# Optimization experiments

Hardware: AMD Instinct MI355X
Metric: run time of the kernel (lower is better)

## Reference

```python
import jax, jax.numpy as jnp
import numpy as np

B, N, T, D, E, M = 8, 512, 64, 128, 32, 3


def _norm(v):
    return v / jnp.clip(jnp.linalg.norm(v, axis=-1, keepdims=True), 1e-12)


def setup_inputs() -> dict:
    key = jax.random.key(0)
    ks = jax.random.split(key, 14)
    s = 0.05
    x = jax.random.normal(ks[0], (B, N, T, 1), jnp.float32)
    # set_prior: binarized adjacency + self loops, row-normalized
    a = (jax.random.uniform(ks[1], (N, N)) > 0.95).astype(jnp.float32) + jnp.eye(N, dtype=jnp.float32)
    prior = a / jnp.clip(a.sum(1, keepdims=True), 1e-8)
    # orthogonal queries, as in torch __init__ (QR of zero-padded randn)
    rng = np.random.default_rng(0)
    qs = []
    for _ in range(M):
        pad = np.zeros((D, D), np.float32)
        pad[:E] = rng.standard_normal((E, D)).astype(np.float32) * 0.1
        q, _ = np.linalg.qr(pad)
        qs.append(q[:E])
    return {
        "x": x,
        "prior": prior,
        "proj_W": jax.random.normal(ks[2], (D, 1), jnp.float32) * s,
        "proj_b": jnp.zeros((D,), jnp.float32),
        "W_ih": jax.random.normal(ks[3], (3 * D, D), jnp.float32) * s,
        "W_hh": jax.random.normal(ks[4], (3 * D, D), jnp.float32) * s,
        "b_ih": jnp.zeros((3 * D,), jnp.float32),
        "b_hh": jnp.zeros((3 * D,), jnp.float32),
        "space_W": jax.random.normal(ks[5], (M, D, D), jnp.float32) * s,
        "space_b": jnp.zeros((M, D), jnp.float32),
        "router_W": jax.random.normal(ks[6], (M, 2 * D), jnp.float32) * s,
        "router_b": jnp.zeros((M,), jnp.float32),
        "out_W": jax.random.normal(ks[7], (1, D), jnp.float32) * s,
        "out_b": jnp.zeros((1,), jnp.float32),
        "prior_logit": jnp.array(1.0, jnp.float32),
        "queries": jnp.asarray(np.stack(qs)),  # [M, E, D]
    }


def reference(x, prior, proj_W, proj_b, W_ih, W_hh, b_ih, b_hh,
              space_W, space_b, router_W, router_b, out_W, out_b,
              prior_logit, queries):
    b, n, t, _ = x.shape
    d = proj_b.shape[0]
    m, e, _ = queries.shape
    # proj(x.permute(0,2,1,3)).reshape(B*N, T, D)  (faithful reshape of [B,T,N,D])
    hp = jnp.transpose(x, (0, 2, 1, 3)) @ proj_W.T + proj_b  # [B,T,N,D]
    seq = hp.reshape(b * n, t, d)
    xs = jnp.swapaxes(seq, 0, 1)  # [T, BN, D]

    def gru_step(h, xt):
        gi = xt @ W_ih.T + b_ih
        gh = h @ W_hh.T + b_hh
        ir, iz, i_n = jnp.split(gi, 3, axis=-1)
        hr, hz, h_n = jnp.split(gh, 3, axis=-1)
        r = jax.nn.sigmoid(ir + hr)
        z = jax.nn.sigmoid(iz + hz)
        ng = jnp.tanh(i_n + r * h_n)
        return (1.0 - z) * ng + z * h, None

    h, _ = jax.lax.scan(gru_step, jnp.zeros((b * n, d), x.dtype), xs)
    h = h.reshape(b, n, d)

    stats = jnp.concatenate([h.mean(1), jnp.std(h, axis=1, ddof=1)], axis=-1)  # torch std is unbiased
    probs = jax.nn.softmax(stats @ router_W.T + router_b, axis=-1)  # [B,M]

    z_prior = jnp.einsum('ij,bjd->bid', prior, h)

    hs = _norm(jnp.einsum('bnd,mkd->bmnk', h, space_W) + space_b[None, :, None, :])  # [B,M,N,D]
    q = _norm(queries)  # [M,E,D]
    scores = jnp.einsum('bmnd,med->bmen', hs, q)  # [B,M,E,N] (topk over N axis)
    k = min(n, max(4, int(n * 0.05)))
    vals, idx = jax.lax.top_k(scores, k)  # [B,M,E,k]
    w = jax.nn.softmax(vals / 0.7, axis=-1)
    H = jnp.zeros((b, m, e, n), h.dtype).at[
        jnp.arange(b)[:, None, None, None],
        jnp.arange(m)[None, :, None, None],
        jnp.arange(e)[None, None, :, None],
        idx,
    ].set(w)  # [B,M,E,N], transposed layout of torch's [B,N,E]

    Hmix = jnp.einsum('bmen,bm->ben', H, probs)  # [B,E,N] == torch Hmix^T
    edge = jnp.einsum('ben,bnd->bed', Hmix, h)   # Hmix^T @ h
    z_learn = jnp.einsum('ben,bed->bnd', Hmix, edge)  # Hmix @ edge

    alpha = jax.nn.sigmoid(prior_logit)
    out = (alpha * z_prior + (1.0 - alpha) * z_learn) @ out_W.T + out_b  # [B,N,1]
    return out.squeeze(-1), probs
```

## Files before the change

### kernel.cpp

```cpp
#include <hip/hip_runtime.h>
#include <math.h>

#define OFF_U      0
#define OFF_C      384
#define OFF_QWHI   768
#define OFF_QWLO   6912
#define OFF_H      13056
#define OFF_PROBS  537344
#define OFF_HV     537376
#define OFF_SCORES 541472
#define OFF_HMIX   934688
#define OFF_WHI    1066016
#define OFF_SHI    1115168
#define OFF_SLO    1139744
#define OFF_STATS  1164320
#define OFF_EV     1229856
#define OFF_QB     1230112

typedef short bf16x8 __attribute__((ext_vector_type(8)));
typedef float f32x4 __attribute__((ext_vector_type(4)));

union U8 { unsigned short s[8]; bf16x8 v; uint4 u4; };

__device__ __forceinline__ unsigned short bf16_rtn(float f) {
  unsigned int u = __float_as_uint(f);
  return (unsigned short)((u + 0x7FFFu + ((u >> 16) & 1u)) >> 16);
}
__device__ __forceinline__ float bf16_f(unsigned short h) {
  return __uint_as_float(((unsigned int)h) << 16);
}

__global__ __launch_bounds__(256) void prep_kernel(const float* __restrict__ Wih,
                                                   const float* __restrict__ projW,
                                                   const float* __restrict__ projb,
                                                   const float* __restrict__ bih,
                                                   const float* __restrict__ queries,
                                                   const float* __restrict__ Whh,
                                                   const float* __restrict__ spaceW,
                                                   const float* __restrict__ spaceb,
                                                   float* __restrict__ ws) {
  const int bid = blockIdx.x, tid = threadIdx.x;
  const int wave = tid >> 6, lane = tid & 63;
  if (bid < 96) {
    int r = bid * 4 + wave;
    float w0 = Wih[r * 128 + lane], w1 = Wih[r * 128 + 64 + lane];
    float u = w0 * projW[lane] + w1 * projW[64 + lane];
    float c = w0 * projb[lane] + w1 * projb[64 + lane];
    for (int off = 32; off; off >>= 1) {
      u += __shfl_xor(u, off);
      c += __shfl_xor(c, off);
    }
    if (lane == 0) {
      ws[OFF_U + r] = u;
      ws[OFF_C + r] = c + bih[r];
    }
  } else if (bid < 112) {
    unsigned short* WHI = (unsigned short*)(ws + OFF_WHI);
    int base = (bid - 96) * 3072;
    for (int i = tid; i < 3072; i += 256)
      WHI[base + i] = bf16_rtn(Whh[base + i]);
  } else if (bid < 128) {
    unsigned short* SHI = (unsigned short*)(ws + OFF_SHI);
    unsigned short* SLO = (unsigned short*)(ws + OFF_SLO);
    int base = (bid - 112) * 3072;
    for (int i = tid; i < 3072; i += 256) {
      float w = spaceW[base + i];
      unsigned short hi = bf16_rtn(w);
      SHI[base + i] = hi;
      SLO[base + i] = bf16_rtn(w - bf16_f(hi));
    }
  } else if (bid < 224) {
    int qi = bid - 128;
    int m = qi >> 5, e = qi & 31;
    __shared__ float invS, qdS;
    const float* qrow = queries + (m * 32 + e) * 128;
    if (wave == 0) {
      float v0 = qrow[lane], v1 = qrow[64 + lane];
      float ss = v0 * v0 + v1 * v1;
      for (int off = 32; off; off >>= 1) ss += __shfl_xor(ss, off);
      if (lane == 0) invS = 1.f / fmaxf(sqrtf(ss), 1e-12f);
    } else if (wave == 1) {
      float v = qrow[lane] * spaceb[m * 128 + lane] +
                qrow[64 + lane] * spaceb[m * 128 + 64 + lane];
      for (int off = 32; off; off >>= 1) v += __shfl_xor(v, off);
      if (lane == 0) qdS = v;
    }
    __syncthreads();
    if (tid < 128) {
      int din = tid;
      float acc = 0.f;
      for (int dout = 0; dout < 128; ++dout)
        acc += qrow[dout] * spaceW[m * 16384 + dout * 128 + din];
      acc *= invS;
      unsigned short hi = bf16_rtn(acc);
      ((unsigned short*)(ws + OFF_QWHI))[(m * 32 + e) * 128 + din] = hi;
      ((unsigned short*)(ws + OFF_QWLO))[(m * 32 + e) * 128 + din] =
          bf16_rtn(acc - bf16_f(hi));
    }
    if (tid == 255) ws[OFF_QB + m * 32 + e] = qdS * invS;
  } else {
    ws[OFF_EV + tid] = 0.f;
  }
}

__global__ __launch_bounds__(512, 2) void gru_kernel(const float* __restrict__ x,
                                                     const float* __restrict__ bhh,
                                                     const float* __restrict__ outW,
                                                     float* __restrict__ ws) {
  __shared__ __align__(16) unsigned short hB[2][16 * 17 * 8];
  __shared__ float xsAll[16 * 65];
  __shared__ float hFin[16 * 132];

  const int tid = threadIdx.x, wave = tid >> 6, lane = tid & 63;
  const int q = lane >> 4, s15 = lane & 15;
  const int d = wave * 16 + s15;
  const unsigned short* WHI = (const unsigned short*)(ws + OFF_WHI);

  {
    float4 z4 = make_float4(0.f, 0.f, 0.f, 0.f);
    float4* hm4 = (float4*)(ws + OFF_HMIX);
    if (tid < 128) hm4[blockIdx.x * 128 + tid] = z4;
  }

  bf16x8 Bh[3][4];
#pragma unroll
  for (int t = 0; t < 3; ++t) {
    int row = (wave + 8 * t) * 16 + s15;
#pragma unroll
    for (int c = 0; c < 4; ++c)
      Bh[t][c] = *(const bf16x8*)&WHI[row * 128 + c * 32 + q * 8];
  }
  const float ur = ws[OFF_U + d],       uz = ws[OFF_U + 128 + d], un = ws[OFF_U + 256 + d];
  const float cr = ws[OFF_C + d] + bhh[d];
  const float cz = ws[OFF_C + 128 + d] + bhh[128 + d];
  const float cn = ws[OFF_C + 256 + d];
  const float bj2 = bhh[256 + d];

  const int seq0 = blockIdx.x * 16;
  for (int i = tid; i < 1024; i += 512) {
    int s = i >> 6, tt = i & 63;
    int r = (seq0 + s) * 64 + tt;
    xsAll[s * 65 + tt] = x[((r >> 15) * 512 + (r & 511)) * 64 + ((r >> 9) & 63)];
  }
  for (int i = tid; i < 2176; i += 512) hB[0][i] = 0;
  __syncthreads();

  float hreg[4] = {0.f, 0.f, 0.f, 0.f};
  const int g = d >> 3, e = d & 7;

  for (int t = 0; t < 64; ++t) {
    const int rb = t & 1, wb = rb ^ 1;
    f32x4 acc0 = {0.f, 0.f, 0.f, 0.f};
    f32x4 acc1 = {0.f, 0.f, 0.f, 0.f};
    f32x4 acc2 = {0.f, 0.f, 0.f, 0.f};
#pragma unroll
    for (int c = 0; c < 4; ++c) {
      bf16x8 A = *(const bf16x8*)&hB[rb][((c * 4 + q) * 17 + s15) * 8];
      acc0 = __builtin_amdgcn_mfma_f32_16x16x32_bf16(A, Bh[0][c], acc0, 0, 0, 0);
      acc1 = __builtin_amdgcn_mfma_f32_16x16x32_bf16(A, Bh[1][c], acc1, 0, 0, 0);
      acc2 = __builtin_amdgcn_mfma_f32_16x16x32_bf16(A, Bh[2][c], acc2, 0, 0, 0);
    }
    float xsv[4];
#pragma unroll
    for (int r = 0; r < 4; ++r) xsv[r] = xsAll[(q * 4 + r) * 65 + t];
#pragma unroll
    for (int r = 0; r < 4; ++r) {
      int s = q * 4 + r;
      float gr = fmaf(xsv[r], ur, cr + acc0[r]);
      float gz = fmaf(xsv[r], uz, cz + acc1[r]);
      float gn = fmaf(xsv[r], un, cn);
      float hn = acc2[r] + bj2;
      float rr = __builtin_amdgcn_rcpf(1.f + __expf(-gr));
      float zm = __builtin_amdgcn_rcpf(1.f + __expf(gz));
      float a = fmaf(rr, hn, gn);
      float ng = 1.f - 2.f * __builtin_amdgcn_rcpf(__expf(2.f * a) + 1.f);
      float hv = fmaf(zm, ng - hreg[r], hreg[r]);
      hreg[r] = hv;
      hB[wb][(g * 17 + s) * 8 + e] = bf16_rtn(hv);
    }
    __syncthreads();
  }

#pragma unroll
  for (int r = 0; r < 4; ++r) hFin[(q * 4 + r) * 132 + d] = hreg[r];
  __syncthreads();
  float* h_out = ws + OFF_H;
#pragma unroll
  for (int p = 0; p < 4; ++p) {
    int item = tid + p * 512;
    int s = item >> 7, dd = item & 127;
    h_out[(seq0 + s) * 128 + dd] = hFin[s * 132 + dd];
  }
  for (int s = wave * 2; s < wave * 2 + 2; ++s) {
    float a = hFin[s * 132 + lane] * outW[lane] + hFin[s * 132 + 64 + lane] * outW[64 + lane];
    for (int off = 32; off; off >>= 1) a += __shfl_xor(a, off);
    if (lane == 0) ws[OFF_HV + seq0 + s] = a;
  }
  if (tid < 128) {
    float s = 0.f, q2 = 0.f;
#pragma unroll
    for (int sI = 0; sI < 16; ++sI) {
      float v = hFin[sI * 132 + tid];
      s += v; q2 += v * v;
    }
    ws[OFF_STATS + blockIdx.x * 256 + tid] = s;
    ws[OFF_STATS + blockIdx.x * 256 + 128 + tid] = q2;
  }
}

__global__ __launch_bounds__(256) void scores_kernel(const float* __restrict__ spaceb,
                                                     const float* __restrict__ routerW,
                                                     const float* __restrict__ routerb,
                                                     float* __restrict__ ws,
                                                     float* __restrict__ d_out) {
  const int bid = blockIdx.x;
  const int chunk = bid & 15, m = (bid >> 4) % 3, b = bid / 48;
  const int n0 = chunk * 32;
  const int tid = threadIdx.x, wave = tid >> 6, lane = tid & 63;
  const int q = lane >> 4, s15 = lane & 15;

  __shared__ __align__(16) unsigned short sHi[16 * 33 * 8];
  __shared__ __align__(16) unsigned short sLo[16 * 33 * 8];
  __shared__ float hsL[32 * 132];
  __shared__ float biasL[128];
  __shared__ float invnL[32];
  __shared__ float qbL[32];

  const float* hG = ws + OFF_H;
  const unsigned short* SHI = (const unsigned short*)(ws + OFF_SHI);
  const unsigned short* SLO = (const unsigned short*)(ws + OFF_SLO);
  const unsigned short* QWHI = (const unsigned short*)(ws + OFF_QWHI);
  const unsigned short* QWLO = (const unsigned short*)(ws + OFF_QWLO);

  if (tid < 128) biasL[tid] = spaceb[m * 128 + tid];
  else if (tid < 160) qbL[tid - 128] = ws[OFF_QB + m * 32 + (tid - 128)];
  {
    int nn = tid >> 3, kc = tid & 7;
    const float* row = &hG[(b * 512 + n0 + nn) * 128 + kc * 16];
    U8 ph0, pl0, ph1, pl1;
#pragma unroll
    for (int j = 0; j < 8; ++j) {
      float v = row[j];
      unsigned short hi = bf16_rtn(v);
      ph0.s[j] = hi; pl0.s[j] = bf16_rtn(v - bf16_f(hi));
    }
#pragma unroll
    for (int j = 0; j < 8; ++j) {
      float v = row[8 + j];
      unsigned short hi = bf16_rtn(v);
      ph1.s[j] = hi; pl1.s[j] = bf16_rtn(v - bf16_f(hi));
    }
    int g0 = kc * 2;
    *(uint4*)&sHi[(g0 * 33 + nn) * 8] = ph0.u4;
    *(uint4*)&sLo[(g0 * 33 + nn) * 8] = pl0.u4;
    *(uint4*)&sHi[((g0 + 1) * 33 + nn) * 8] = ph1.u4;
    *(uint4*)&sLo[((g0 + 1) * 33 + nn) * 8] = pl1.u4;
  }
  __syncthreads();

  const int nt = wave >> 1;
  const int half = wave & 1;
  const int dt0 = half * 4;
  f32x4 acc[4] = {{0.f,0.f,0.f,0.f},{0.f,0.f,0.f,0.f},{0.f,0.f,0.f,0.f},{0.f,0.f,0.f,0.f}};
  f32x4 accS = {0.f, 0.f, 0.f, 0.f};
#pragma unroll
  for (int c = 0; c < 4; ++c) {
    bf16x8 Ahi = *(const bf16x8*)&sHi[((c * 4 + q) * 33 + nt * 16 + s15) * 8];
    bf16x8 Alo = *(const bf16x8*)&sLo[((c * 4 + q) * 33 + nt * 16 + s15) * 8];
#pragma unroll
    for (int i = 0; i < 4; ++i) {
      int row = m * 16384 + ((dt0 + i) * 16 + s15) * 128 + c * 32 + q * 8;
      bf16x8 Bhi = *(const bf16x8*)&SHI[row];
      bf16x8 Blo = *(const bf16x8*)&SLO[row];
      acc[i] = __builtin_amdgcn_mfma_f32_16x16x32_bf16(Ahi, Bhi, acc[i], 0, 0, 0);
      acc[i] = __builtin_amdgcn_mfma_f32_16x16x32_bf16(Alo, Bhi, acc[i], 0, 0, 0);
      acc[i] = __builtin_amdgcn_mfma_f32_16x16x32_bf16(Ahi, Blo, acc[i], 0, 0, 0);
    }
    {
      int row = (m * 32 + half * 16 + s15) * 128 + c * 32 + q * 8;
      bf16x8 Qhi = *(const bf16x8*)&QWHI[row];
      bf16x8 Qlo = *(const bf16x8*)&QWLO[row];
      accS = __builtin_amdgcn_mfma_f32_16x16x32_bf16(Ahi, Qhi, accS, 0, 0, 0);
      accS = __builtin_amdgcn_mfma_f32_16x16x32_bf16(Alo, Qhi, accS, 0, 0, 0);
      accS = __builtin_amdgcn_mfma_f32_16x16x32_bf16(Ahi, Qlo, accS, 0, 0, 0);
    }
  }
#pragma unroll
  for (int i = 0; i < 4; ++i) {
    int dcol = (dt0 + i) * 16 + s15;
    float bb = biasL[dcol];
#pragma unroll
    for (int r = 0; r < 4; ++r)
      hsL[(nt * 16 + q * 4 + r) * 132 + dcol] = acc[i][r] + bb;
  }
  __syncthreads();

  {
    int n = tid >> 3, kc = tid & 7;
    float ss = 0.f;
#pragma unroll
    for (int d4 = 0; d4 < 4; ++d4) {
      float4 v = *(const float4*)&hsL[n * 132 + kc * 16 + d4 * 4];
      ss += v.x * v.x + v.y * v.y + v.z * v.z + v.w * v.w;
    }
    ss += __shfl_xor(ss, 1); ss += __shfl_xor(ss, 2); ss += __shfl_xor(ss, 4);
    if (kc == 0) invnL[n] = 1.f / fmaxf(sqrtf(ss), 1e-12f);
  }
  __syncthreads();

  {
    int e = half * 16 + s15;
    float qb = qbL[e];
    int nb = nt * 16 + q * 4;
    float4 o;
    o.x = (accS[0] + qb) * invnL[nb + 0];
    o.y = (accS[1] + qb) * invnL[nb + 1];
    o.z = (accS[2] + qb) * invnL[nb + 2];
    o.w = (accS[3] + qb) * invnL[nb + 3];
    *(float4*)&ws[OFF_SCORES + ((b * 3 + m) * 32 + e) * 512 + n0 + nb] = o;
  }

  if ((bid % 48) == 0) {
    __syncthreads();
    float* st = hsL;
    float* lgS = hsL + 256;
    if (tid < 128) {
      float s = 0.f, q2 = 0.f;
      const float* base = ws + OFF_STATS + b * 32 * 256;
      for (int j = 0; j < 32; ++j) {
        s += base[j * 256 + tid];
        q2 += base[j * 256 + 128 + tid];
      }
      float mean = s * (1.f / 512.f);
      float var = (q2 - 512.f * mean * mean) * (1.f / 511.f);
      st[tid] = mean;
      st[128 + tid] = sqrtf(fmaxf(var, 0.f));
    }
    __syncthreads();
    if (tid < 3) {
      float acc2 = routerb[tid];
      for (int k = 0; k < 256; ++k) acc2 += st[k] * routerW[tid * 256 + k];
      lgS[tid] = acc2;
    }
    __syncthreads();
    if (tid == 0) {
      float mx = fmaxf(lgS[0], fmaxf(lgS[1], lgS[2]));
      float e0 = expf(lgS[0] - mx), e1 = expf(lgS[1] - mx), e2 = expf(lgS[2] - mx);
      float inv = 1.f / (e0 + e1 + e2);
      ws[OFF_PROBS + b * 3 + 0] = e0 * inv;
      ws[OFF_PROBS + b * 3 + 1] = e1 * inv;
      ws[OFF_PROBS + b * 3 + 2] = e2 * inv;
      d_out[4096 + b * 3 + 0] = e0 * inv;
      d_out[4096 + b * 3 + 1] = e1 * inv;
      d_out[4096 + b * 3 + 2] = e2 * inv;
    }
  }
}

__global__ __launch_bounds__(256) void topk_kernel(float* __restrict__ ws) {
  const int row0 = blockIdx.x * 4;
  const int b = row0 / 96;
  const int tid = threadIdx.x, wave = tid >> 6, lane = tid & 63;
  __shared__ float hvL[512];
  hvL[tid] = ws[OFF_HV + b * 512 + tid];
  hvL[256 + tid] = ws[OFF_HV + b * 512 + 256 + tid];
  __syncthreads();

  int row = row0 + wave;
  int m = (row / 32) % 3, e = row & 31;
  const float* sc = ws + OFF_SCORES + row * 512;
  float prob = ws[OFF_PROBS + b * 3 + m];

  float v[8];
#pragma unroll
  for (int j = 0; j < 8; ++j) v[j] = sc[j * 64 + lane];

  float selv = 0.f; int seli = 0; float maxv = 0.f;
  for (int it = 0; it < 25; ++it) {
    float bv = v[0]; int bj = 0;
#pragma unroll
    for (int j = 1; j < 8; ++j)
      if (v[j] > bv) { bv = v[j]; bj = j; }
    int bidx = bj * 64 + lane;
    for (int off = 32; off; off >>= 1) {
      float ov = __shfl_xor(bv, off);
      int oi = __shfl_xor(bidx, off);
      if (ov > bv || (ov == bv && oi < bidx)) { bv = ov; bidx = oi; }
    }
    if (lane == (bidx & 63)) v[bidx >> 6] = -INFINITY;
    if (it == 0) maxv = bv;
    if (lane == it) { selv = bv; seli = bidx; }
  }
  float ex = (lane < 25) ? __expf((selv - maxv) * (1.f / 0.7f)) : 0.f;
  float den = ex;
  for (int off = 32; off; off >>= 1) den += __shfl_xor(den, off);
  float w = prob * ex / den;
  if (lane < 25)
    atomicAdd(&ws[OFF_HMIX + (b * 32 + e) * 512 + seli], w);
  float evc = (lane < 25) ? w * hvL[seli] : 0.f;
  for (int off = 32; off; off >>= 1) evc += __shfl_xor(evc, off);
  if (lane == 0) atomicAdd(&ws[OFF_EV + b * 32 + e], evc);
}

__global__ __launch_bounds__(512) void final_kernel(const float* __restrict__ prior,
                                                    const float* __restrict__ outb,
                                                    const float* __restrict__ plog,
                                                    float* __restrict__ ws,
                                                    float* __restrict__ d_out) {
  const int bid = blockIdx.x;
  const int b = bid >> 4, ch = bid & 15;
  const int tid = threadIdx.x, wave = tid >> 6, lane = tid & 63;
  __shared__ float hvL[512], evL[32];
  hvL[tid] = ws[OFF_HV + b * 512 + tid];
  if (tid < 32) evL[tid] = ws[OFF_EV + b * 32 + tid];
  __syncthreads();
  float alpha = 1.f / (1.f + expf(-plog[0]));
  float ob = outb[0];
#pragma unroll
  for (int i = 0; i < 4; ++i) {
    int n = ch * 32 + wave * 4 + i;
    const float* pr = prior + n * 512;
    float s1 = 0.f;
#pragma unroll
    for (int j = 0; j < 8; ++j) s1 += pr[j * 64 + lane] * hvL[j * 64 + lane];
    float s2 = 0.f;
    if (lane < 32) s2 = ws[OFF_HMIX + (b * 32 + lane) * 512 + n] * evL[lane];
    float a = alpha * s1 + (1.f - alpha) * s2;
    for (int off = 32; off; off >>= 1) a += __shfl_xor(a, off);
    if (lane == 0) d_out[b * 512 + n] = a + ob;
  }
}

extern "C" void kernel_launch(void* const* d_in, const int* in_sizes, int n_in,
                              void* d_out, int out_size, void* d_ws, size_t ws_size,
                              hipStream_t stream) {
  const float* x       = (const float*)d_in[0];
  const float* prior   = (const float*)d_in[1];
  const float* projW   = (const float*)d_in[2];
  const float* projb   = (const float*)d_in[3];
  const float* Wih     = (const float*)d_in[4];
  const float* Whh     = (const float*)d_in[5];
  const float* bih     = (const float*)d_in[6];
  const float* bhh     = (const float*)d_in[7];
  const float* spaceW  = (const float*)d_in[8];
  const float* spaceb  = (const float*)d_in[9];
  const float* routerW = (const float*)d_in[10];
  const float* routerb = (const float*)d_in[11];
  const float* outW    = (const float*)d_in[12];
  const float* outb    = (const float*)d_in[13];
  const float* plog    = (const float*)d_in[14];
  const float* queries = (const float*)d_in[15];
  float* ws  = (float*)d_ws;
  float* out = (float*)d_out;

  prep_kernel<<<225, 256, 0, stream>>>(Wih, projW, projb, bih, queries, Whh,
                                       spaceW, spaceb, ws);
  gru_kernel<<<256, 512, 0, stream>>>(x, bhh, outW, ws);
  scores_kernel<<<384, 256, 0, stream>>>(spaceb, routerW, routerb, ws, out);
  topk_kernel<<<192, 256, 0, stream>>>(ws);
  final_kernel<<<128, 512, 0, stream>>>(prior, outb, plog, ws, out);
}
```

Before: 174.9 us.

## Fuse scores, topk and final into one kernel with grid-wide spin barriers

Merges the scores, top-k and final kernels into a single persistent 384-block kernel that separates the phases with atomic-counter spin barriers instead of kernel launches. The spaceW splitting, query-weight precompute and EV/sync-counter zeroing move out of the prep kernel into extra blocks appended to the GRU launch, so prep shrinks to the GRU-weight work. The aim is to cut launch gaps and inter-kernel drain time. The spin barriers assume all 384 blocks are co-resident, which risks deadlock if they are not, and they add atomic polling cost.

```diff
diff --git a/kernel.cpp b/kernel.cpp
--- a/kernel.cpp
+++ b/kernel.cpp
@@ -7,6 +7,7 @@
 #define OFF_QWLO   6912
 #define OFF_H      13056
 #define OFF_PROBS  537344
+#define OFF_SYNC   537368
 #define OFF_HV     537376
 #define OFF_SCORES 541472
 #define OFF_HMIX   934688
@@ -30,14 +31,23 @@
   return __uint_as_float(((unsigned int)h) << 16);
 }
 
+__device__ __forceinline__ void spin_sync(unsigned* ctr, unsigned target, int tid) {
+  __threadfence();
+  __syncthreads();
+  if (tid == 0) {
+    __hip_atomic_fetch_add(ctr, 1u, __ATOMIC_ACQ_REL, __HIP_MEMORY_SCOPE_AGENT);
+    while (__hip_atomic_load(ctr, __ATOMIC_ACQUIRE, __HIP_MEMORY_SCOPE_AGENT) < target)
+      __builtin_amdgcn_s_sleep(4);
+  }
+  __syncthreads();
+  __threadfence();
+}
+
 __global__ __launch_bounds__(256) void prep_kernel(const float* __restrict__ Wih,
                                                    const float* __restrict__ projW,
                                                    const float* __restrict__ projb,
                                                    const float* __restrict__ bih,
-                                                   const float* __restrict__ queries,
                                                    const float* __restrict__ Whh,
-                                                   const float* __restrict__ spaceW,
-                                                   const float* __restrict__ spaceb,
                                                    float* __restrict__ ws) {
   const int bid = blockIdx.x, tid = threadIdx.x;
   const int wave = tid >> 6, lane = tid & 63;
@@ -54,64 +64,76 @@
       ws[OFF_U + r] = u;
       ws[OFF_C + r] = c + bih[r];
     }
-  } else if (bid < 112) {
+  } else {
     unsigned short* WHI = (unsigned short*)(ws + OFF_WHI);
     int base = (bid - 96) * 3072;
     for (int i = tid; i < 3072; i += 256)
       WHI[base + i] = bf16_rtn(Whh[base + i]);
-  } else if (bid < 128) {
-    unsigned short* SHI = (unsigned short*)(ws + OFF_SHI);
-    unsigned short* SLO = (unsigned short*)(ws + OFF_SLO);
-    int base = (bid - 112) * 3072;
-    for (int i = tid; i < 3072; i += 256) {
-      float w = spaceW[base + i];
-      unsigned short hi = bf16_rtn(w);
-      SHI[base + i] = hi;
-      SLO[base + i] = bf16_rtn(w - bf16_f(hi));
-    }
-  } else if (bid < 224) {
-    int qi = bid - 128;
-    int m = qi >> 5, e = qi & 31;
-    __shared__ float invS, qdS;
-    const float* qrow = queries + (m * 32 + e) * 128;
-    if (wave == 0) {
-      float v0 = qrow[lane], v1 = qrow[64 + lane];
-      float ss = v0 * v0 + v1 * v1;
-      for (int off = 32; off; off >>= 1) ss += __shfl_xor(ss, off);
-      if (lane == 0) invS = 1.f / fmaxf(sqrtf(ss), 1e-12f);
-    } else if (wave == 1) {
-      float v = qrow[lane] * spaceb[m * 128 + lane] +
-                qrow[64 + lane] * spaceb[m * 128 + 64 + lane];
-      for (int off = 32; off; off >>= 1) v += __shfl_xor(v, off);
-      if (lane == 0) qdS = v;
-    }
-    __syncthreads();
-    if (tid < 128) {
-      int din = tid;
-      float acc = 0.f;
-      for (int dout = 0; dout < 128; ++dout)
-        acc += qrow[dout] * spaceW[m * 16384 + dout * 128 + din];
-      acc *= invS;
-      unsigned short hi = bf16_rtn(acc);
-      ((unsigned short*)(ws + OFF_QWHI))[(m * 32 + e) * 128 + din] = hi;
-      ((unsigned short*)(ws + OFF_QWLO))[(m * 32 + e) * 128 + din] =
-          bf16_rtn(acc - bf16_f(hi));
-    }
-    if (tid == 255) ws[OFF_QB + m * 32 + e] = qdS * invS;
-  } else {
-    ws[OFF_EV + tid] = 0.f;
   }
 }
 
 __global__ __launch_bounds__(512, 2) void gru_kernel(const float* __restrict__ x,
                                                      const float* __restrict__ bhh,
                                                      const float* __restrict__ outW,
+                                                     const float* __restrict__ spaceW,
+                                                     const float* __restrict__ spaceb,
+                                                     const float* __restrict__ queries,
                                                      float* __restrict__ ws) {
   __shared__ __align__(16) unsigned short hB[2][16 * 17 * 8];
   __shared__ float xsAll[16 * 65];
   __shared__ float hFin[16 * 132];
+  __shared__ float invS, qdS;
 
   const int tid = threadIdx.x, wave = tid >> 6, lane = tid & 63;
+
+  if (blockIdx.x >= 256) {
+    const int xb = blockIdx.x - 256;
+    if (xb < 16) {
+      unsigned short* SHI = (unsigned short*)(ws + OFF_SHI);
+      unsigned short* SLO = (unsigned short*)(ws + OFF_SLO);
+      int base = xb * 3072;
+      for (int i = tid; i < 3072; i += 512) {
+        float w = spaceW[base + i];
+        unsigned short hi = bf16_rtn(w);
+        SHI[base + i] = hi;
+        SLO[base + i] = bf16_rtn(w - bf16_f(hi));
+      }
+    } else if (xb < 112) {
+      int qi = xb - 16;
+      int m = qi >> 5, e = qi & 31;
+      const float* qrow = queries + (m * 32 + e) * 128;
+      if (wave == 0) {
+        float v0 = qrow[lane], v1 = qrow[64 + lane];
+        float ss = v0 * v0 + v1 * v1;
+        for (int off = 32; off; off >>= 1) ss += __shfl_xor(ss, off);
+        if (lane == 0) invS = 1.f / fmaxf(sqrtf(ss), 1e-12f);
+      } else if (wave == 1) {
+        float v = qrow[lane] * spaceb[m * 128 + lane] +
+                  qrow[64 + lane] * spaceb[m * 128 + 64 + lane];
+        for (int off = 32; off; off >>= 1) v += __shfl_xor(v, off);
+        if (lane == 0) qdS = v;
+      }
+      __syncthreads();
+      if (tid < 128) {
+        int din = tid;
+        float acc = 0.f;
+        for (int dout = 0; dout < 128; ++dout)
+          acc += qrow[dout] * spaceW[m * 16384 + dout * 128 + din];
+        acc *= invS;
+        unsigned short hi = bf16_rtn(acc);
+        ((unsigned short*)(ws + OFF_QWHI))[(m * 32 + e) * 128 + din] = hi;
+        ((unsigned short*)(ws + OFF_QWLO))[(m * 32 + e) * 128 + din] =
+            bf16_rtn(acc - bf16_f(hi));
+      }
+      if (tid == 0) ws[OFF_QB + m * 32 + e] = qdS * invS;
+    } else {
+      if (tid < 256) ws[OFF_EV + tid] = 0.f;
+      if (tid == 256) ((unsigned*)(ws + OFF_SYNC))[0] = 0u;
+      if (tid == 257) ((unsigned*)(ws + OFF_SYNC))[1] = 0u;
+    }
+    return;
+  }
+
   const int q = lane >> 4, s15 = lane & 15;
   const int d = wave * 16 + s15;
   const unsigned short* WHI = (const unsigned short*)(ws + OFF_WHI);
@@ -208,14 +230,15 @@
   }
 }
 
-__global__ __launch_bounds__(256) void scores_kernel(const float* __restrict__ spaceb,
-                                                     const float* __restrict__ routerW,
-                                                     const float* __restrict__ routerb,
-                                                     float* __restrict__ ws,
-                                                     float* __restrict__ d_out) {
+__global__ __launch_bounds__(256) void megatail_kernel(const float* __restrict__ spaceb,
+                                                       const float* __restrict__ routerW,
+                                                       const float* __restrict__ routerb,
+                                                       const float* __restrict__ prior,
+                                                       const float* __restrict__ outb,
+                                                       const float* __restrict__ plog,
+                                                       float* __restrict__ ws,
+                                                       float* __restrict__ d_out) {
   const int bid = blockIdx.x;
-  const int chunk = bid & 15, m = (bid >> 4) % 3, b = bid / 48;
-  const int n0 = chunk * 32;
   const int tid = threadIdx.x, wave = tid >> 6, lane = tid & 63;
   const int q = lane >> 4, s15 = lane & 15;
 
@@ -226,208 +249,204 @@
   __shared__ float invnL[32];
   __shared__ float qbL[32];
 
-  const float* hG = ws + OFF_H;
-  const unsigned short* SHI = (const unsigned short*)(ws + OFF_SHI);
-  const unsigned short* SLO = (const unsigned short*)(ws + OFF_SLO);
-  const unsigned short* QWHI = (const unsigned short*)(ws + OFF_QWHI);
-  const unsigned short* QWLO = (const unsigned short*)(ws + OFF_QWLO);
-
-  if (tid < 128) biasL[tid] = spaceb[m * 128 + tid];
-  else if (tid < 160) qbL[tid - 128] = ws[OFF_QB + m * 32 + (tid - 128)];
+  unsigned* ctr = (unsigned*)(ws + OFF_SYNC);
+
   {
-    int nn = tid >> 3, kc = tid & 7;
-    const float* row = &hG[(b * 512 + n0 + nn) * 128 + kc * 16];
-    U8 ph0, pl0, ph1, pl1;
-#pragma unroll
-    for (int j = 0; j < 8; ++j) {
-      float v = row[j];
-      unsigned short hi = bf16_rtn(v);
-      ph0.s[j] = hi; pl0.s[j] = bf16_rtn(v - bf16_f(hi));
-    }
-#pragma unroll
-    for (int j = 0; j < 8; ++j) {
-      float v = row[8 + j];
-      unsigned short hi = bf16_rtn(v);
-      ph1.s[j] = hi; pl1.s[j] = bf16_rtn(v - bf16_f(hi));
-    }
-    int g0 = kc * 2;
-    *(uint4*)&sHi[(g0 * 33 + nn) * 8] = ph0.u4;
-    *(uint4*)&sLo[(g0 * 33 + nn) * 8] = pl0.u4;
-    *(uint4*)&sHi[((g0 + 1) * 33 + nn) * 8] = ph1.u4;
-    *(uint4*)&sLo[((g0 + 1) * 33 + nn) * 8] = pl1.u4;
-  }
-  __syncthreads();
-
-  const int nt = wave >> 1;
-  const int half = wave & 1;
-  const int dt0 = half * 4;
-  f32x4 acc[4] = {{0.f,0.f,0.f,0.f},{0.f,0.f,0.f,0.f},{0.f,0.f,0.f,0.f},{0.f,0.f,0.f,0.f}};
-  f32x4 accS = {0.f, 0.f, 0.f, 0.f};
-#pragma unroll
-  for (int c = 0; c < 4; ++c) {
-    bf16x8 Ahi = *(const bf16x8*)&sHi[((c * 4 + q) * 33 + nt * 16 + s15) * 8];
-    bf16x8 Alo = *(const bf16x8*)&sLo[((c * 4 + q) * 33 + nt * 16 + s15) * 8];
+    const int chunk = bid & 15, m = (bid >> 4) % 3, b = bid / 48;
+    const int n0 = chunk * 32;
+    const float* hG = ws + OFF_H;
+    const unsigned short* SHI = (const unsigned short*)(ws + OFF_SHI);
+    const unsigned short* SLO = (const unsigned short*)(ws + OFF_SLO);
+    const unsigned short* QWHI = (const unsigned short*)(ws + OFF_QWHI);
+    const unsigned short* QWLO = (const unsigned short*)(ws + OFF_QWLO);
+
+    if (tid < 128) biasL[tid] = spaceb[m * 128 + tid];
+    else if (tid < 160) qbL[tid - 128] = ws[OFF_QB + m * 32 + (tid - 128)];
+    {
+      int nn = tid >> 3, kc = tid & 7;
+      const float* row = &hG[(b * 512 + n0 + nn) * 128 + kc * 16];
+      U8 ph0, pl0, ph1, pl1;
+#pragma unroll
+      for (int j = 0; j < 8; ++j) {
+        float v = row[j];
+        unsigned short hi = bf16_rtn(v);
+        ph0.s[j] = hi; pl0.s[j] = bf16_rtn(v - bf16_f(hi));
+      }
+#pragma unroll
+      for (int j = 0; j < 8; ++j) {
+        float v = row[8 + j];
+        unsigned short hi = bf16_rtn(v);
+        ph1.s[j] = hi; pl1.s[j] = bf16_rtn(v - bf16_f(hi));
+      }
+      int g0 = kc * 2;
+      *(uint4*)&sHi[(g0 * 33 + nn) * 8] = ph0.u4;
+      *(uint4*)&sLo[(g0 * 33 + nn) * 8] = pl0.u4;
+      *(uint4*)&sHi[((g0 + 1) * 33 + nn) * 8] = ph1.u4;
+      *(uint4*)&sLo[((g0 + 1) * 33 + nn) * 8] = pl1.u4;
+    }
+    __syncthreads();
+
+    const int nt = wave >> 1;
+    const int half = wave & 1;
+    const int dt0 = half * 4;
+    f32x4 acc[4] = {{0.f,0.f,0.f,0.f},{0.f,0.f,0.f,0.f},{0.f,0.f,0.f,0.f},{0.f,0.f,0.f,0.f}};
+    f32x4 accS = {0.f, 0.f, 0.f, 0.f};
+#pragma unroll
+    for (int c = 0; c < 4; ++c) {
+      bf16x8 Ahi = *(const bf16x8*)&sHi[((c * 4 + q) * 33 + nt * 16 + s15) * 8];
+      bf16x8 Alo = *(const bf16x8*)&sLo[((c * 4 + q) * 33 + nt * 16 + s15) * 8];
+#pragma unroll
+      for (int i = 0; i < 4; ++i) {
+        int row = m * 16384 + ((dt0 + i) * 16 + s15) * 128 + c * 32 + q * 8;
+        bf16x8 Bhi = *(const bf16x8*)&SHI[row];
+        bf16x8 Blo = *(const bf16x8*)&SLO[row];
+        acc[i] = __builtin_amdgcn_mfma_f32_16x16x32_bf16(Ahi, Bhi, acc[i], 0, 0, 0);
+        acc[i] = __builtin_amdgcn_mfma_f32_16x16x32_bf16(Alo, Bhi, acc[i], 0, 0, 0);
+        acc[i] = __builtin_amdgcn_mfma_f32_16x16x32_bf16(Ahi, Blo, acc[i], 0, 0, 0);
+      }
+      {
+        int row = (m * 32 + half * 16 + s15) * 128 + c * 32 + q * 8;
+        bf16x8 Qhi = *(const bf16x8*)&QWHI[row];
+        bf16x8 Qlo = *(const bf16x8*)&QWLO[row];
+        accS = __builtin_amdgcn_mfma_f32_16x16x32_bf16(Ahi, Qhi, accS, 0, 0, 0);
+        accS = __builtin_amdgcn_mfma_f32_16x16x32_bf16(Alo, Qhi, accS, 0, 0, 0);
+        accS = __builtin_amdgcn_mfma_f32_16x16x32_bf16(Ahi, Qlo, accS, 0, 0, 0);
+      }
+    }
 #pragma unroll
     for (int i = 0; i < 4; ++i) {
-      int row = m * 16384 + ((dt0 + i) * 16 + s15) * 128 + c * 32 + q * 8;
-      bf16x8 Bhi = *(const bf16x8*)&SHI[row];
-      bf16x8 Blo = *(const bf16x8*)&SLO[row];
-      acc[i] = __builtin_amdgcn_mfma_f32_16x16x32_bf16(Ahi, Bhi, acc[i], 0, 0, 0);
-      acc[i] = __builtin_amdgcn_mfma_f32_16x16x32_bf16(Alo, Bhi, acc[i], 0, 0, 0);
-      acc[i] = __builtin_amdgcn_mfma_f32_16x16x32_bf16(Ahi, Blo, acc[i], 0, 0, 0);
-    }
+      int dcol = (dt0 + i) * 16 + s15;
+      float bb = biasL[dcol];
+#pragma unroll
+      for (int r = 0; r < 4; ++r)
+        hsL[(nt * 16 + q * 4 + r) * 132 + dcol] = acc[i][r] + bb;
+    }
+    __syncthreads();
+
     {
-      int row = (m * 32 + half * 16 + s15) * 128 + c * 32 + q * 8;
-      bf16x8 Qhi = *(const bf16x8*)&QWHI[row];
-      bf16x8 Qlo = *(const bf16x8*)&QWLO[row];
-      accS = __builtin_amdgcn_mfma_f32_16x16x32_bf16(Ahi, Qhi, accS, 0, 0, 0);
-      accS = __builtin_amdgcn_mfma_f32_16x16x32_bf16(Alo, Qhi, accS, 0, 0, 0);
-      accS = __builtin_amdgcn_mfma_f32_16x16x32_bf16(Ahi, Qlo, accS, 0, 0, 0);
-    }
-  }
-#pragma unroll
-  for (int i = 0; i < 4; ++i) {
-    int dcol = (dt0 + i) * 16 + s15;
-    float bb = biasL[dcol];
-#pragma unroll
-    for (int r = 0; r < 4; ++r)
-      hsL[(nt * 16 + q * 4 + r) * 132 + dcol] = acc[i][r] + bb;
-  }
-  __syncthreads();
+      int n = tid >> 3, kc = tid & 7;
+      float ss = 0.f;
+#pragma unroll
+      for (int d4 = 0; d4 < 4; ++d4) {
+        float4 v = *(const float4*)&hsL[n * 132 + kc * 16 + d4 * 4];
+        ss += v.x * v.x + v.y * v.y + v.z * v.z + v.w * v.w;
+      }
+      ss += __shfl_xor(ss, 1); ss += __shfl_xor(ss, 2); ss += __shfl_xor(ss, 4);
+      if (kc == 0) invnL[n] = 1.f / fmaxf(sqrtf(ss), 1e-12f);
+    }
+    __syncthreads();
+
+    {
+      int e = half * 16 + s15;
+      float qb = qbL[e];
+      int nb = nt * 16 + q * 4;
+      float4 o;
+      o.x = (accS[0] + qb) * invnL[nb + 0];
+      o.y = (accS[1] + qb) * invnL[nb + 1];
+      o.z = (accS[2] + qb) * invnL[nb + 2];
+      o.w = (accS[3] + qb) * invnL[nb + 3];
+      *(float4*)&ws[OFF_SCORES + ((b * 3 + m) * 32 + e) * 512 + n0 + nb] = o;
+    }
+
+    if ((bid % 48) == 0) {
+      __syncthreads();
+      float* st = hsL;
+      float* lgS = hsL + 256;
+      if (tid < 128) {
+        float s = 0.f, q2 = 0.f;
+        const float* base = ws + OFF_STATS + b * 32 * 256;
+        for (int j = 0; j < 32; ++j) {
+          s += base[j * 256 + tid];
+          q2 += base[j * 256 + 128 + tid];
+        }
+        float mean = s * (1.f / 512.f);
+        float var = (q2 - 512.f * mean * mean) * (1.f / 511.f);
+        st[tid] = mean;
+        st[128 + tid] = sqrtf(fmaxf(var, 0.f));
+      }
+      __syncthreads();
+      if (tid < 3) {
+        float acc2 = routerb[tid];
+        for (int k = 0; k < 256; ++k) acc2 += st[k] * routerW[tid * 256 + k];
+        lgS[tid] = acc2;
+      }
+      __syncthreads();
+      if (tid == 0) {
+        float mx = fmaxf(lgS[0], fmaxf(lgS[1], lgS[2]));
+        float e0 = expf(lgS[0] - mx), e1 = expf(lgS[1] - mx), e2 = expf(lgS[2] - mx);
+        float inv = 1.f / (e0 + e1 + e2);
+        ws[OFF_PROBS + b * 3 + 0] = e0 * inv;
+        ws[OFF_PROBS + b * 3 + 1] = e1 * inv;
+        ws[OFF_PROBS + b * 3 + 2] = e2 * inv;
+        d_out[4096 + b * 3 + 0] = e0 * inv;
+        d_out[4096 + b * 3 + 1] = e1 * inv;
+        d_out[4096 + b * 3 + 2] = e2 * inv;
+      }
+    }
+  }
+
+  spin_sync(&ctr[0], 384u, tid);
 
   {
-    int n = tid >> 3, kc = tid & 7;
-    float ss = 0.f;
-#pragma unroll
-    for (int d4 = 0; d4 < 4; ++d4) {
-      float4 v = *(const float4*)&hsL[n * 132 + kc * 16 + d4 * 4];
-      ss += v.x * v.x + v.y * v.y + v.z * v.z + v.w * v.w;
-    }
-    ss += __shfl_xor(ss, 1); ss += __shfl_xor(ss, 2); ss += __shfl_xor(ss, 4);
-    if (kc == 0) invnL[n] = 1.f / fmaxf(sqrtf(ss), 1e-12f);
-  }
-  __syncthreads();
+    const int b = bid / 48;
+    for (int i = tid; i < 512; i += 256) hsL[i] = ws[OFF_HV + b * 512 + i];
+    __syncthreads();
+    if (wave < 2) {
+      int row = bid * 2 + wave;
+      int m = (row / 32) % 3, e = row & 31;
+      const float* sc = ws + OFF_SCORES + row * 512;
+      float prob = ws[OFF_PROBS + b * 3 + m];
+      float v[8];
+#pragma unroll
+      for (int j = 0; j < 8; ++j) v[j] = sc[j * 64 + lane];
+      float selv = 0.f; int seli = 0; float maxv = 0.f;
+      for (int it = 0; it < 25; ++it) {
+        float bv = v[0]; int bj = 0;
+#pragma unroll
+        for (int j = 1; j < 8; ++j)
+          if (v[j] > bv) { bv = v[j]; bj = j; }
+        int bidx = bj * 64 + lane;
+        for (int off = 32; off; off >>= 1) {
+          float ov = __shfl_xor(bv, off);
+          int oi = __shfl_xor(bidx, off);
+          if (ov > bv || (ov == bv && oi < bidx)) { bv = ov; bidx = oi; }
+        }
+        if (lane == (bidx & 63)) v[bidx >> 6] = -INFINITY;
+        if (it == 0) maxv = bv;
+        if (lane == it) { selv = bv; seli = bidx; }
+      }
+      float ex = (lane < 25) ? __expf((selv - maxv) * (1.f / 0.7f)) : 0.f;
+      float den = ex;
+      for (int off = 32; off; off >>= 1) den += __shfl_xor(den, off);
+      float w = prob * ex / den;
+      if (lane < 25)
+        atomicAdd(&ws[OFF_HMIX + (b * 32 + e) * 512 + seli], w);
+      float evc = (lane < 25) ? w * hsL[seli] : 0.f;
+      for (int off = 32; off; off >>= 1) evc += __shfl_xor(evc, off);
+      if (lane == 0) atomicAdd(&ws[OFF_EV + b * 32 + e], evc);
+    }
+  }
+
+  spin_sync(&ctr[1], 384u, tid);
 
   {
-    int e = half * 16 + s15;
-    float qb = qbL[e];
-    int nb = nt * 16 + q * 4;
-    float4 o;
-    o.x = (accS[0] + qb) * invnL[nb + 0];
-    o.y = (accS[1] + qb) * invnL[nb + 1];
-    o.z = (accS[2] + qb) * invnL[nb + 2];
-    o.w = (accS[3] + qb) * invnL[nb + 3];
-    *(float4*)&ws[OFF_SCORES + ((b * 3 + m) * 32 + e) * 512 + n0 + nb] = o;
-  }
-
-  if ((bid % 48) == 0) {
-    __syncthreads();
-    float* st = hsL;
-    float* lgS = hsL + 256;
-    if (tid < 128) {
-      float s = 0.f, q2 = 0.f;
-      const float* base = ws + OFF_STATS + b * 32 * 256;
-      for (int j = 0; j < 32; ++j) {
-        s += base[j * 256 + tid];
-        q2 += base[j * 256 + 128 + tid];
-      }
-      float mean = s * (1.f / 512.f);
-      float var = (q2 - 512.f * mean * mean) * (1.f / 511.f);
-      st[tid] = mean;
-      st[128 + tid] = sqrtf(fmaxf(var, 0.f));
-    }
-    __syncthreads();
-    if (tid < 3) {
-      float acc2 = routerb[tid];
-      for (int k = 0; k < 256; ++k) acc2 += st[k] * routerW[tid * 256 + k];
-      lgS[tid] = acc2;
-    }
-    __syncthreads();
-    if (tid == 0) {
-      float mx = fmaxf(lgS[0], fmaxf(lgS[1], lgS[2]));
-      float e0 = expf(lgS[0] - mx), e1 = expf(lgS[1] - mx), e2 = expf(lgS[2] - mx);
-      float inv = 1.f / (e0 + e1 + e2);
-      ws[OFF_PROBS + b * 3 + 0] = e0 * inv;
-      ws[OFF_PROBS + b * 3 + 1] = e1 * inv;
-      ws[OFF_PROBS + b * 3 + 2] = e2 * inv;
-      d_out[4096 + b * 3 + 0] = e0 * inv;
-      d_out[4096 + b * 3 + 1] = e1 * inv;
-      d_out[4096 + b * 3 + 2] = e2 * inv;
-    }
-  }
-}
-
-__global__ __launch_bounds__(256) void topk_kernel(float* __restrict__ ws) {
-  const int row0 = blockIdx.x * 4;
-  const int b = row0 / 96;
-  const int tid = threadIdx.x, wave = tid >> 6, lane = tid & 63;
-  __shared__ float hvL[512];
-  hvL[tid] = ws[OFF_HV + b * 512 + tid];
-  hvL[256 + tid] = ws[OFF_HV + b * 512 + 256 + tid];
-  __syncthreads();
-
-  int row = row0 + wave;
-  int m = (row / 32) % 3, e = row & 31;
-  const float* sc = ws + OFF_SCORES + row * 512;
-  float prob = ws[OFF_PROBS + b * 3 + m];
-
-  float v[8];
-#pragma unroll
-  for (int j = 0; j < 8; ++j) v[j] = sc[j * 64 + lane];
-
-  float selv = 0.f; int seli = 0; float maxv = 0.f;
-  for (int it = 0; it < 25; ++it) {
-    float bv = v[0]; int bj = 0;
-#pragma unroll
-    for (int j = 1; j < 8; ++j)
-      if (v[j] > bv) { bv = v[j]; bj = j; }
-    int bidx = bj * 64 + lane;
-    for (int off = 32; off; off >>= 1) {
-      float ov = __shfl_xor(bv, off);
-      int oi = __shfl_xor(bidx, off);
-      if (ov > bv || (ov == bv && oi < bidx)) { bv = ov; bidx = oi; }
-    }
-    if (lane == (bidx & 63)) v[bidx >> 6] = -INFINITY;
-    if (it == 0) maxv = bv;
-    if (lane == it) { selv = bv; seli = bidx; }
-  }
-  float ex = (lane < 25) ? __expf((selv - maxv) * (1.f / 0.7f)) : 0.f;
-  float den = ex;
-  for (int off = 32; off; off >>= 1) den += __shfl_xor(den, off);
-  float w = prob * ex / den;
-  if (lane < 25)
-    atomicAdd(&ws[OFF_HMIX + (b * 32 + e) * 512 + seli], w);
-  float evc = (lane < 25) ? w * hvL[seli] : 0.f;
-  for (int off = 32; off; off >>= 1) evc += __shfl_xor(evc, off);
-  if (lane == 0) atomicAdd(&ws[OFF_EV + b * 32 + e], evc);
-}
-
-__global__ __launch_bounds__(512) void final_kernel(const float* __restrict__ prior,
-                                                    const float* __restrict__ outb,
-                                                    const float* __restrict__ plog,
-                                                    float* __restrict__ ws,
-                                                    float* __restrict__ d_out) {
-  const int bid = blockIdx.x;
-  const int b = bid >> 4, ch = bid & 15;
-  const int tid = threadIdx.x, wave = tid >> 6, lane = tid & 63;
-  __shared__ float hvL[512], evL[32];
-  hvL[tid] = ws[OFF_HV + b * 512 + tid];
-  if (tid < 32) evL[tid] = ws[OFF_EV + b * 32 + tid];
-  __syncthreads();
-  float alpha = 1.f / (1.f + expf(-plog[0]));
-  float ob = outb[0];
-#pragma unroll
-  for (int i = 0; i < 4; ++i) {
-    int n = ch * 32 + wave * 4 + i;
-    const float* pr = prior + n * 512;
-    float s1 = 0.f;
-#pragma unroll
-    for (int j = 0; j < 8; ++j) s1 += pr[j * 64 + lane] * hvL[j * 64 + lane];
-    float s2 = 0.f;
-    if (lane < 32) s2 = ws[OFF_HMIX + (b * 32 + lane) * 512 + n] * evL[lane];
-    float a = alpha * s1 + (1.f - alpha) * s2;
-    for (int off = 32; off; off >>= 1) a += __shfl_xor(a, off);
-    if (lane == 0) d_out[b * 512 + n] = a + ob;
+    float alpha = 1.f / (1.f + expf(-plog[0]));
+    float ob = outb[0];
+    const int gw = bid * 4 + wave;
+    for (int row = gw; row < 4096; row += 1536) {
+      int b = row >> 9, n = row & 511;
+      const float* hv = ws + OFF_HV + b * 512;
+      const float* pr = prior + n * 512;
+      float s1 = 0.f;
+#pragma unroll
+      for (int j = 0; j < 8; ++j) s1 += pr[j * 64 + lane] * hv[j * 64 + lane];
+      float s2 = 0.f;
+      if (lane < 32)
+        s2 = ws[OFF_HMIX + (b * 32 + lane) * 512 + n] * ws[OFF_EV + b * 32 + lane];
+      float a = alpha * s1 + (1.f - alpha) * s2;
+      for (int off = 32; off; off >>= 1) a += __shfl_xor(a, off);
+      if (lane == 0) d_out[row] = a + ob;
+    }
   }
 }
 
@@ -453,10 +472,8 @@
   float* ws  = (float*)d_ws;
   float* out = (float*)d_out;
 
-  prep_kernel<<<225, 256, 0, stream>>>(Wih, projW, projb, bih, queries, Whh,
-                                       spaceW, spaceb, ws);
-  gru_kernel<<<256, 512, 0, stream>>>(x, bhh, outW, ws);
-  scores_kernel<<<384, 256, 0, stream>>>(spaceb, routerW, routerb, ws, out);
-  topk_kernel<<<192, 256, 0, stream>>>(ws);
-  final_kernel<<<128, 512, 0, stream>>>(prior, outb, plog, ws, out);
-}
+  prep_kernel<<<112, 256, 0, stream>>>(Wih, projW, projb, bih, Whh, ws);
+  gru_kernel<<<369, 512, 0, stream>>>(x, bhh, outW, spaceW, spaceb, queries, ws);
+  megatail_kernel<<<384, 256, 0, stream>>>(spaceb, routerW, routerb, prior,
+                                           outb, plog, ws, out);
+}
```

Result: slower. 361.5 us (+106.7%).
